# Performance work log

Hardware: AMD Instinct MI355X
Metric: run time of the kernel (lower is better)

## Reference

```python
import jax, jax.numpy as jnp
import numpy as np

N_NODES = 50000
N_EDGES = 800000
HIDDEN = 128
NUM_LAYERS = 3
NEG_SLOPE = 0.2  # PyG GATConv default leaky_relu slope


def setup_inputs() -> dict:
    key = jax.random.key(0)
    ks = jax.random.split(key, 10)
    d = HIDDEN
    glorot = 1.0 / np.sqrt(d)
    inp = {
        "x": jax.random.normal(ks[0], (N_NODES, d), dtype=jnp.float32),
        "edge_index": jax.random.randint(ks[1], (2, N_EDGES), 0, N_NODES, dtype=jnp.int32),
        "edge_mask": jax.random.uniform(ks[2], (N_EDGES,), dtype=jnp.float32),
        # GATConv params (heads=1)
        "W_gat": jax.random.normal(ks[3], (d, d), dtype=jnp.float32) * glorot,
        "a_src": jax.random.normal(ks[4], (d,), dtype=jnp.float32) * glorot,
        "a_dst": jax.random.normal(ks[5], (d,), dtype=jnp.float32) * glorot,
        "b_gat": jnp.zeros((d,), dtype=jnp.float32),
        # Stacked GCNConv params
        "W_gcn": jax.random.normal(ks[6], (NUM_LAYERS, d, d), dtype=jnp.float32) * glorot,
        "b_gcn": jnp.zeros((NUM_LAYERS, d), dtype=jnp.float32),
    }
    return inp


def _seg_softmax(e, seg, n):
    m = jax.ops.segment_max(e, seg, num_segments=n)
    p = jnp.exp(e - m[seg])
    s = jax.ops.segment_sum(p, seg, num_segments=n)
    return p / s[seg]


def reference(x, edge_index, edge_mask, W_gat, a_src, a_dst, b_gat, W_gcn, b_gcn):
    N = x.shape[0]
    loops = jnp.arange(N, dtype=edge_index.dtype)
    src = jnp.concatenate([edge_index[0], loops])  # [E+N] with self loops
    dst = jnp.concatenate([edge_index[1], loops])

    # --- GATConv (heads=1, add_self_loops=True); edge_attr ignored (edge_dim=None) ---
    xp = x @ W_gat                                      # [N, d]
    e = jax.nn.leaky_relu((xp @ a_src)[src] + (xp @ a_dst)[dst], NEG_SLOPE)
    alpha = _seg_softmax(e, dst, N)                     # segment softmax over incoming edges
    h = jax.ops.segment_sum(alpha[:, None] * xp[src], dst, num_segments=N) + b_gat

    # --- GCN normalization with edge_mask as edge_weight (self-loop weight = 1) ---
    w = jnp.concatenate([edge_mask, jnp.ones((N,), dtype=edge_mask.dtype)])
    deg = jax.ops.segment_sum(w, dst, num_segments=N)
    dinv = jnp.where(deg > 0, jax.lax.rsqrt(jnp.maximum(deg, 1e-12)), 0.0)
    norm = dinv[src] * w * dinv[dst]                    # [E+N]

    outs = [h]
    for l in range(NUM_LAYERS):
        z = outs[-1] @ W_gcn[l]                         # [N, d]
        z = jax.ops.segment_sum(norm[:, None] * z[src], dst, num_segments=N) + b_gcn[l]
        outs.append(jax.nn.relu(z))

    # JumpingKnowledge 'max': elementwise max over layer outputs
    return jnp.max(jnp.stack(outs, axis=0), axis=0)
```

## Files before the change

### kernel.cpp

```cpp
#include <hip/hip_runtime.h>

#define HIDDEN 128
#define NEG_SLOPE 0.2f
#define P_SORT 256

typedef unsigned short ushort_t;
typedef __attribute__((ext_vector_type(8))) short short8;
typedef __attribute__((ext_vector_type(4))) float floatx4;

static inline size_t align_up(size_t x, size_t a){ return (x + a - 1) & ~(a - 1); }

__device__ __forceinline__ ushort_t f2b(float f){
  unsigned u = __float_as_uint(f);
  unsigned r = (u + 0x7FFFu + ((u >> 16) & 1u)) >> 16;
  return (ushort_t)r;
}

__device__ __forceinline__ float b2f(ushort_t u){
  return __uint_as_float(((unsigned)u) << 16);
}

__device__ __forceinline__ void fma8(float* acc, uint4 v, float a){
  acc[0] += a * __uint_as_float(v.x << 16);
  acc[1] += a * __uint_as_float(v.x & 0xFFFF0000u);
  acc[2] += a * __uint_as_float(v.y << 16);
  acc[3] += a * __uint_as_float(v.y & 0xFFFF0000u);
  acc[4] += a * __uint_as_float(v.z << 16);
  acc[5] += a * __uint_as_float(v.z & 0xFFFF0000u);
  acc[6] += a * __uint_as_float(v.w << 16);
  acc[7] += a * __uint_as_float(v.w & 0xFFFF0000u);
}

__device__ __forceinline__ uint4 pack8(const float* f){
  uint4 u;
  u.x = (unsigned)f2b(f[0]) | ((unsigned)f2b(f[1]) << 16);
  u.y = (unsigned)f2b(f[2]) | ((unsigned)f2b(f[3]) << 16);
  u.z = (unsigned)f2b(f[4]) | ((unsigned)f2b(f[5]) << 16);
  u.w = (unsigned)f2b(f[6]) | ((unsigned)f2b(f[7]) << 16);
  return u;
}


__global__ __launch_bounds__(256) void k_b1cnt(const int* __restrict__ dst,
                                               int* __restrict__ bcnt,
                                               int E, int epb, int nbkt){
  __shared__ unsigned c[256];
  int t = threadIdx.x;
  c[t] = 0;
  __syncthreads();
  int e0 = blockIdx.x * epb;
  int e1 = min(E, e0 + epb);
  for (int e = e0 + t; e < e1; e += 256) atomicAdd(&c[dst[e] >> 8], 1u);
  __syncthreads();
  if (t < nbkt) bcnt[t * P_SORT + blockIdx.x] = (int)c[t];
}

__global__ void k_scan1(const int* __restrict__ in, int* __restrict__ incl,
                        int* __restrict__ blockSums, int M){
  __shared__ int sd[256];
  int t = threadIdx.x;
  int i = blockIdx.x*256 + t;
  int v = (i < M) ? in[i] : 0;
  sd[t] = v; __syncthreads();
  for (int off = 1; off < 256; off <<= 1){
    int add = (t >= off) ? sd[t-off] : 0;
    __syncthreads();
    sd[t] += add;
    __syncthreads();
  }
  if (i < M) incl[i] = sd[t];
  if (t == 255) blockSums[blockIdx.x] = sd[255];
}

__global__ void k_scan2(const int* __restrict__ blockSums, int* __restrict__ blockOffs, int nb){
  __shared__ int sd[256];
  __shared__ int carry;
  int t = threadIdx.x;
  if (t == 0) carry = 0;
  __syncthreads();
  for (int base = 0; base < nb; base += 256){
    int i = base + t;
    int v = (i < nb) ? blockSums[i] : 0;
    sd[t] = v; __syncthreads();
    for (int off = 1; off < 256; off <<= 1){
      int add = (t >= off) ? sd[t-off] : 0;
      __syncthreads();
      sd[t] += add;
      __syncthreads();
    }
    if (i < nb) blockOffs[i] = carry + sd[t] - v;
    __syncthreads();
    if (t == 0) carry += sd[255];
    __syncthreads();
  }
}

__global__ __launch_bounds__(256) void k_b1place(const int* __restrict__ src,
                                                 const int* __restrict__ dst,
                                                 const float* __restrict__ w,
                                                 const int* __restrict__ incl,
                                                 const int* __restrict__ bcnt,
                                                 const int* __restrict__ blockOffs,
                                                 int2* __restrict__ tpw,
                                                 int E, int epb, int nbkt){
  __shared__ int base_[256];
  __shared__ unsigned c[256];
  int t = threadIdx.x;
  c[t] = 0;
  if (t < nbkt){
    int idx = t * P_SORT + blockIdx.x;
    base_[t] = incl[idx] - bcnt[idx] + blockOffs[t];
  }
  __syncthreads();
  int e0 = blockIdx.x * epb;
  int e1 = min(E, e0 + epb);
  for (int e = e0 + t; e < e1; e += 256){
    int d = dst[e];
    int b = d >> 8;
    unsigned r = atomicAdd(&c[b], 1u);
    int pos = base_[b] + (int)r;
    tpw[pos] = make_int2((int)((unsigned)src[e] | ((unsigned)(d & 255) << 16)),
                         __float_as_int(w[e]));
  }
}

__global__ __launch_bounds__(256) void k_b2(const int2* __restrict__ tpw,
                                            const int* __restrict__ blockOffs,
                                            int2* __restrict__ col_sw,
                                            int* __restrict__ rowp,
                                            float* __restrict__ dinv,
                                            int N, int E, int nbkt){
  __shared__ int cnt[4096];
  __shared__ int tsum[256];
  __shared__ float wsum[256];
  int b = blockIdx.x, t = threadIdx.x;
  int e0 = blockOffs[b];
  int e1 = (b + 1 < nbkt) ? blockOffs[b + 1] : E;
  #pragma unroll
  for (int i = 0; i < 16; i++) cnt[t*16 + i] = 0;
  wsum[t] = 0.f;
  __syncthreads();
  for (int e = e0 + t; e < e1; e += 256){
    int2 pw = tpw[e];
    unsigned dl = ((unsigned)pw.x >> 16) & 255u;
    unsigned s  = ((unsigned)pw.x & 0xFFFFu) >> 12;
    atomicAdd(&cnt[(dl << 4) | s], 1);
  }
  __syncthreads();
  int loc[16]; int run = 0;
  #pragma unroll
  for (int i = 0; i < 16; i++){ loc[i] = run; run += cnt[t*16 + i]; }
  tsum[t] = run;
  __syncthreads();
  for (int off = 1; off < 256; off <<= 1){
    int add = (t >= off) ? tsum[t-off] : 0;
    __syncthreads();
    tsum[t] += add;
    __syncthreads();
  }
  int base = tsum[t] - run;
  #pragma unroll
  for (int i = 0; i < 16; i++) cnt[t*16 + i] = base + loc[i];
  int node = b*256 + t;
  if (node < N) rowp[node] = e0 + base;
  if (b == 0 && t == 0) rowp[N] = E;
  __syncthreads();
  for (int e = e0 + t; e < e1; e += 256){
    int2 pw = tpw[e];
    unsigned dl = ((unsigned)pw.x >> 16) & 255u;
    unsigned srcv = (unsigned)pw.x & 0xFFFFu;
    unsigned s = srcv >> 12;
    int pos = e0 + atomicAdd(&cnt[(dl << 4) | s], 1);
    col_sw[pos] = make_int2((int)srcv, pw.y);
    atomicAdd(&wsum[dl], __int_as_float(pw.y));
  }
  __syncthreads();
  if (node < N) dinv[node] = rsqrtf(wsum[t] + 1.0f);
}


__global__ void k_cast_w(const float* __restrict__ Wg, const float* __restrict__ Wc,
                         ushort_t* __restrict__ Wt){
  int i = blockIdx.x*256 + threadIdx.x;
  int mat = i >> 14, idx = i & 16383;
  int k = idx >> 7, n = idx & 127;
  float v = (mat == 0) ? Wg[idx] : Wc[(mat-1)*16384 + idx];
  Wt[mat*16384 + n*128 + k] = f2b(v);
}

__global__ __launch_bounds__(128) void k_gemm1(const float* __restrict__ Ain,
                                               const ushort_t* __restrict__ Wt,
                                               ushort_t* __restrict__ C,
                                               const float* __restrict__ a_src,
                                               const float* __restrict__ a_dst,
                                               const float* __restrict__ dinv,
                                               float2* __restrict__ attr,
                                               float* __restrict__ sdst, int M){
  int wave = threadIdx.x >> 6, l = threadIdx.x & 63;
  int q = l >> 4, lm = l & 15;
  int rowBase = blockIdx.x*64 + wave*32;
  floatx4 acc[2][8];
  #pragma unroll
  for (int mt = 0; mt < 2; mt++)
    #pragma unroll
    for (int nt = 0; nt < 8; nt++) acc[mt][nt] = (floatx4){0.f,0.f,0.f,0.f};

  #pragma unroll
  for (int kc = 0; kc < 4; kc++){
    int k0 = kc*32 + q*8;
    short8 a[2];
    #pragma unroll
    for (int mt = 0; mt < 2; mt++){
      long r = rowBase + mt*16 + lm;
      if (r < M){
        const float* ap = Ain + r*128 + k0;
        float4 u = *(const float4*)ap;
        float4 v = *(const float4*)(ap + 4);
        short8 tv;
        tv[0]=(short)f2b(u.x); tv[1]=(short)f2b(u.y); tv[2]=(short)f2b(u.z); tv[3]=(short)f2b(u.w);
        tv[4]=(short)f2b(v.x); tv[5]=(short)f2b(v.y); tv[6]=(short)f2b(v.z); tv[7]=(short)f2b(v.w);
        a[mt] = tv;
      } else a[mt] = (short8){0,0,0,0,0,0,0,0};
    }
    #pragma unroll
    for (int nt = 0; nt < 8; nt++){
      short8 b = *(const short8*)(Wt + (nt*16 + lm)*128 + k0);
      acc[0][nt] = __builtin_amdgcn_mfma_f32_16x16x32_bf16(a[0], b, acc[0][nt], 0, 0, 0);
      acc[1][nt] = __builtin_amdgcn_mfma_f32_16x16x32_bf16(a[1], b, acc[1][nt], 0, 0, 0);
    }
  }
  #pragma unroll
  for (int mt = 0; mt < 2; mt++){
    #pragma unroll
    for (int r = 0; r < 4; r++){
      long row = rowBase + mt*16 + q*4 + r;
      if (row < M){
        #pragma unroll
        for (int nt = 0; nt < 8; nt++)
          C[row*128 + nt*16 + lm] = f2b(acc[mt][nt][r]);
      }
    }
  }
  float as8[8], ad8[8];
  #pragma unroll
  for (int nt = 0; nt < 8; nt++){ as8[nt] = a_src[nt*16 + lm]; ad8[nt] = a_dst[nt*16 + lm]; }
  #pragma unroll
  for (int mt = 0; mt < 2; mt++){
    #pragma unroll
    for (int r = 0; r < 4; r++){
      float ps = 0.f, pd = 0.f;
      #pragma unroll
      for (int nt = 0; nt < 8; nt++){
        ps += acc[mt][nt][r] * as8[nt];
        pd += acc[mt][nt][r] * ad8[nt];
      }
      #pragma unroll
      for (int off = 1; off <= 8; off <<= 1){
        ps += __shfl_xor(ps, off, 64);
        pd += __shfl_xor(pd, off, 64);
      }
      long row = rowBase + mt*16 + q*4 + r;
      if (lm == 0 && row < M){
        attr[row] = make_float2(ps, dinv[row]);
        sdst[row] = pd;
      }
    }
  }
}

__global__ __launch_bounds__(256) void k_agg0(const ushort_t* __restrict__ feat,
                                              const int* __restrict__ rowp,
                                              const int2* __restrict__ col_sw,
                                              int2* __restrict__ col_en,
                                              int2* __restrict__ col_ea,
                                              const float2* __restrict__ attr,
                                              const float* __restrict__ sdst_,
                                              const float* __restrict__ bias,
                                              ushort_t* __restrict__ out, int N){
  int n = blockIdx.x*4 + (threadIdx.x >> 6);
  if (n >= N) return;
  int l = threadIdx.x & 63;
  int rs = rowp[n], re = rowp[n+1];
  float2 an = attr[n];
  float sdd = sdst_[n];
  float es = an.x + sdd;
  es = (es >= 0.f) ? es : NEG_SLOPE*es;
  float pself = __expf(es);
  float ps = 0.f;
  for (int j = rs + l; j < re; j += 64){
    int2 sw = col_sw[j];
    float w = __int_as_float(sw.y);
    float2 a = attr[sw.x];
    col_en[j] = make_int2(sw.x, __float_as_int(a.y * w * an.y));
    float ee = a.x + sdd;
    ee = (ee >= 0.f) ? ee : NEG_SLOPE*ee;
    float pe = __expf(ee);
    ps += pe;
    col_ea[j] = make_int2(sw.x, __float_as_int(pe));
  }
  #pragma unroll
  for (int off = 32; off >= 1; off >>= 1) ps += __shfl_xor(ps, off, 64);
  float inv = 1.f / (ps + pself);

  int sub = l >> 4, q = l & 15;
  const uint4* f16 = (const uint4*)feat;
  float acc[8] = {0.f,0.f,0.f,0.f,0.f,0.f,0.f,0.f};
  for (int base = rs; base < re; base += 24){
    int2 p[6]; float a[6];
    #pragma unroll
    for (int j = 0; j < 6; j++){
      int e = base + sub + 4*j;
      int cc = min(e, re-1);
      p[j] = col_ea[cc];
      a[j] = (e < re) ? __int_as_float(p[j].y) : 0.f;
    }
    uint4 v[6];
    #pragma unroll
    for (int j = 0; j < 6; j++) v[j] = f16[(size_t)p[j].x*16 + q];
    #pragma unroll
    for (int j = 0; j < 6; j++) fma8(acc, v[j], a[j]);
  }
  #pragma unroll
  for (int j = 0; j < 8; j++){
    acc[j] += __shfl_xor(acc[j], 16, 64);
    acc[j] += __shfl_xor(acc[j], 32, 64);
  }
  if (sub == 0){
    #pragma unroll
    for (int j = 0; j < 8; j++) acc[j] *= inv;
    uint4 v = f16[(size_t)n*16 + q];
    fma8(acc, v, pself * inv);
    float4 b0 = ((const float4*)bias)[q*2];
    float4 b1 = ((const float4*)bias)[q*2 + 1];
    acc[0]+=b0.x; acc[1]+=b0.y; acc[2]+=b0.z; acc[3]+=b0.w;
    acc[4]+=b1.x; acc[5]+=b1.y; acc[6]+=b1.z; acc[7]+=b1.w;
    ((uint4*)out)[(size_t)n*16 + q] = pack8(acc);
  }
}

template<int MODE>
__global__ __launch_bounds__(256) void k_fagg(const ushort_t* __restrict__ feat,
                                              const int* __restrict__ rowp,
                                              const int2* __restrict__ col_en,
                                              const float* __restrict__ dinv,
                                              const ushort_t* __restrict__ Wl,
                                              const float* __restrict__ bias,
                                              ushort_t* __restrict__ out,
                                              const ushort_t* __restrict__ j0,
                                              const ushort_t* __restrict__ j1,
                                              const ushort_t* __restrict__ j2,
                                              float* __restrict__ yout, int N){
  __shared__ ushort_t At[16][136];
  int wave = threadIdx.x >> 6, l = threadIdx.x & 63;
  int sub = l >> 4, q = l & 15;
  const uint4* f16 = (const uint4*)feat;
  int tile = blockIdx.x * 16;

  for (int i = 0; i < 4; i++){
    int row = wave*4 + i;
    int n = tile + row;
    int rs = 0, re = 0;
    if (n < N){ rs = rowp[n]; re = rowp[n+1]; }
    float acc[8] = {0.f,0.f,0.f,0.f,0.f,0.f,0.f,0.f};
    for (int base = rs; base < re; base += 24){
      int2 p[6]; float a[6];
      #pragma unroll
      for (int j = 0; j < 6; j++){
        int e = base + sub + 4*j;
        int cc = min(e, re-1);
        p[j] = col_en[cc];
        a[j] = (e < re) ? __int_as_float(p[j].y) : 0.f;
      }
      uint4 v[6];
      #pragma unroll
      for (int j = 0; j < 6; j++) v[j] = f16[(size_t)p[j].x*16 + q];
      #pragma unroll
      for (int j = 0; j < 6; j++) fma8(acc, v[j], a[j]);
    }
    #pragma unroll
    for (int j = 0; j < 8; j++){
      acc[j] += __shfl_xor(acc[j], 16, 64);
      acc[j] += __shfl_xor(acc[j], 32, 64);
    }
    if (sub == 0){
      if (n < N){
        float di = dinv[n];
        uint4 v = f16[(size_t)n*16 + q];
        fma8(acc, v, di*di);
      }
      *(uint4*)&At[row][q*8] = pack8(acc);
    }
  }
  __syncthreads();

  floatx4 co[2];
  co[0] = (floatx4){0.f,0.f,0.f,0.f};
  co[1] = (floatx4){0.f,0.f,0.f,0.f};
  #pragma unroll
  for (int kc = 0; kc < 4; kc++){
    int k0 = kc*32 + sub*8;
    short8 a = *(const short8*)&At[q][k0];
    #pragma unroll
    for (int ntl = 0; ntl < 2; ntl++){
      int nt = wave*2 + ntl;
      short8 b = *(const short8*)(Wl + (size_t)(nt*16 + q)*128 + k0);
      co[ntl] = __builtin_amdgcn_mfma_f32_16x16x32_bf16(a, b, co[ntl], 0, 0, 0);
    }
  }
  #pragma unroll
  for (int r = 0; r < 4; r++){
    int row = sub*4 + r;
    int node = tile + row;
    if (node < N){
      #pragma unroll
      for (int ntl = 0; ntl < 2; ntl++){
        int colg = wave*32 + ntl*16 + q;
        float v = co[ntl][r] + bias[colg];
        v = fmaxf(v, 0.f);
        size_t idx = (size_t)node*128 + colg;
        if (MODE == 1){
          out[idx] = f2b(v);
        } else {
          float m = fmaxf(fmaxf(b2f(j0[idx]), b2f(j1[idx])),
                          fmaxf(b2f(j2[idx]), v));
          yout[idx] = m;
        }
      }
    }
  }
}

extern "C" void kernel_launch(void* const* d_in, const int* in_sizes, int n_in,
                              void* d_out, int out_size, void* d_ws, size_t ws_size,
                              hipStream_t stream){
  const float* x      = (const float*)d_in[0];
  const int*   eidx   = (const int*)d_in[1];
  const float* emask  = (const float*)d_in[2];
  const float* W_gat  = (const float*)d_in[3];
  const float* a_src  = (const float*)d_in[4];
  const float* a_dst  = (const float*)d_in[5];
  const float* b_gat  = (const float*)d_in[6];
  const float* W_gcn  = (const float*)d_in[7];
  const float* b_gcn  = (const float*)d_in[8];
  int N = in_sizes[0] / HIDDEN;
  int E = in_sizes[1] / 2;
  const int* src = eidx;
  const int* dst = eidx + E;

  char* p = (char*)d_ws;
  auto carve = [&](size_t bytes)->char*{ char* q = p; p += align_up(bytes, 512); return q; };
  ushort_t* zb   = (ushort_t*)carve((size_t)N*HIDDEN*2);
  ushort_t* h0   = (ushort_t*)carve((size_t)N*HIDDEN*2);
  ushort_t* h1   = (ushort_t*)carve((size_t)N*HIDDEN*2);
  ushort_t* h2   = (ushort_t*)carve((size_t)N*HIDDEN*2);
  ushort_t* Wt   = (ushort_t*)carve((size_t)4*HIDDEN*HIDDEN*2);
  float2* attr   = (float2*)carve((size_t)N*8);
  float* sdst    = (float*)carve((size_t)N*4);
  float* dinv    = (float*)carve((size_t)N*4);
  int*   rowp    = (int*)  carve((size_t)(N+1)*4);
  int2*  col_sw  = (int2*) carve((size_t)E*8);
  int2*  col_en  = (int2*) carve((size_t)E*8);
  int2*  col_ea  = (int2*) carve((size_t)E*8);
  int2*  tpw     = (int2*) carve((size_t)E*8);
  int nbkt = (N + 255) >> 8;
  int M    = nbkt * P_SORT;
  int*   bcnt  = (int*)carve((size_t)M*4);
  int*   incl  = (int*)carve((size_t)M*4);
  int nbs = (M + 255) / 256;
  int*   blockSums = (int*)carve((size_t)nbs*4);
  int*   blockOffs = (int*)carve((size_t)nbs*4);
  (void)ws_size; (void)n_in; (void)out_size;

  int epb = (E + P_SORT - 1) / P_SORT;
  int gb  = (N + 63) / 64;
  int nwb = (N + 3) / 4;
  int nfb = (N + 15) / 16;

  k_b1cnt  <<<P_SORT, 256, 0, stream>>>(dst, bcnt, E, epb, nbkt);
  k_scan1  <<<nbs, 256, 0, stream>>>(bcnt, incl, blockSums, M);
  k_scan2  <<<1,   256, 0, stream>>>(blockSums, blockOffs, nbs);
  k_b1place<<<P_SORT, 256, 0, stream>>>(src, dst, emask, incl, bcnt, blockOffs,
                                        tpw, E, epb, nbkt);
  k_b2     <<<nbkt, 256, 0, stream>>>(tpw, blockOffs, col_sw, rowp, dinv, N, E, nbkt);

  k_cast_w<<<(4*HIDDEN*HIDDEN)/256, 256, 0, stream>>>(W_gat, W_gcn, Wt);

  k_gemm1<<<gb, 128, 0, stream>>>(x, Wt, zb, a_src, a_dst, dinv, attr, sdst, N);

  k_agg0<<<nwb, 256, 0, stream>>>(zb, rowp, col_sw, col_en, col_ea, attr, sdst,
                                  b_gat, h0, N);

  k_fagg<1><<<nfb, 256, 0, stream>>>(h0, rowp, col_en, dinv, Wt + (size_t)1*16384,
                                     b_gcn + 0, h1,
                                     nullptr, nullptr, nullptr, nullptr, N);
  k_fagg<1><<<nfb, 256, 0, stream>>>(h1, rowp, col_en, dinv, Wt + (size_t)2*16384,
                                     b_gcn + 128, h2,
                                     nullptr, nullptr, nullptr, nullptr, N);
  k_fagg<2><<<nfb, 256, 0, stream>>>(h2, rowp, col_en, dinv, Wt + (size_t)3*16384,
                                     b_gcn + 256, nullptr,
                                     h0, h1, h2, (float*)d_out, N);
}
```

Baseline: 340.6 us.

## Quantize gathered node features to int8 with per-row scales for aggregation

Node feature tables that are gathered per edge (the GAT projection and each GCN layer's input) are stored as int8 with a per-row float scale instead of bf16. The scale is folded into the edge weights, so the gather reads half the bytes. The precomputed col_en edge array is dropped: GCN edge weights are rebuilt on the fly from col_sw and the per-node scale, which also folds in dinv. This trades extra scale loads and LDS staging against lower gather bandwidth, and adds quantization error that may break the accuracy tolerance.

Result: slower. 392.8 us (+15.3%).

```diff
diff --git a/kernel.cpp b/kernel.cpp
--- a/kernel.cpp
+++ b/kernel.cpp
@@ -20,15 +20,30 @@
   return __uint_as_float(((unsigned)u) << 16);
 }
 
-__device__ __forceinline__ void fma8(float* acc, uint4 v, float a){
-  acc[0] += a * __uint_as_float(v.x << 16);
-  acc[1] += a * __uint_as_float(v.x & 0xFFFF0000u);
-  acc[2] += a * __uint_as_float(v.y << 16);
-  acc[3] += a * __uint_as_float(v.y & 0xFFFF0000u);
-  acc[4] += a * __uint_as_float(v.z << 16);
-  acc[5] += a * __uint_as_float(v.z & 0xFFFF0000u);
-  acc[6] += a * __uint_as_float(v.w << 16);
-  acc[7] += a * __uint_as_float(v.w & 0xFFFF0000u);
+__device__ __forceinline__ void fma8q(float* acc, uint2 v, float a){
+  int x = (int)v.x, y = (int)v.y;
+  acc[0] += a * (float)((x << 24) >> 24);
+  acc[1] += a * (float)((x << 16) >> 24);
+  acc[2] += a * (float)((x <<  8) >> 24);
+  acc[3] += a * (float)( x        >> 24);
+  acc[4] += a * (float)((y << 24) >> 24);
+  acc[5] += a * (float)((y << 16) >> 24);
+  acc[6] += a * (float)((y <<  8) >> 24);
+  acc[7] += a * (float)( y        >> 24);
+}
+
+__device__ __forceinline__ uint2 packq8(const float* f, float qi){
+  unsigned a = 0, b = 0;
+  int q;
+  q = (int)rintf(f[0]*qi); a |= ((unsigned)q & 255u);
+  q = (int)rintf(f[1]*qi); a |= ((unsigned)q & 255u) << 8;
+  q = (int)rintf(f[2]*qi); a |= ((unsigned)q & 255u) << 16;
+  q = (int)rintf(f[3]*qi); a |= ((unsigned)q & 255u) << 24;
+  q = (int)rintf(f[4]*qi); b |= ((unsigned)q & 255u);
+  q = (int)rintf(f[5]*qi); b |= ((unsigned)q & 255u) << 8;
+  q = (int)rintf(f[6]*qi); b |= ((unsigned)q & 255u) << 16;
+  q = (int)rintf(f[7]*qi); b |= ((unsigned)q & 255u) << 24;
+  uint2 r; r.x = a; r.y = b; return r;
 }
 
 __device__ __forceinline__ uint4 pack8(const float* f){
@@ -190,12 +205,15 @@
 
 __global__ __launch_bounds__(128) void k_gemm1(const float* __restrict__ Ain,
                                                const ushort_t* __restrict__ Wt,
-                                               ushort_t* __restrict__ C,
+                                               unsigned* __restrict__ zq,
+                                               float* __restrict__ sc_z,
                                                const float* __restrict__ a_src,
                                                const float* __restrict__ a_dst,
                                                const float* __restrict__ dinv,
                                                float2* __restrict__ attr,
                                                float* __restrict__ sdst, int M){
+  __shared__ uint4 zq8v[64][8];
+  char (*zq8)[128] = (char(*)[128])zq8v;
   int wave = threadIdx.x >> 6, l = threadIdx.x & 63;
   int q = l >> 4, lm = l & 15;
   int rowBase = blockIdx.x*64 + wave*32;
@@ -233,12 +251,18 @@
   for (int mt = 0; mt < 2; mt++){
     #pragma unroll
     for (int r = 0; r < 4; r++){
+      float rm = 0.f;
+      #pragma unroll
+      for (int nt = 0; nt < 8; nt++) rm = fmaxf(rm, fabsf(acc[mt][nt][r]));
+      #pragma unroll
+      for (int off = 1; off <= 8; off <<= 1) rm = fmaxf(rm, __shfl_xor(rm, off, 64));
+      float qi = (rm > 0.f) ? 127.f/rm : 0.f;
+      int lrow = wave*32 + mt*16 + q*4 + r;
+      #pragma unroll
+      for (int nt = 0; nt < 8; nt++)
+        zq8[lrow][nt*16 + lm] = (char)(int)rintf(acc[mt][nt][r]*qi);
       long row = rowBase + mt*16 + q*4 + r;
-      if (row < M){
-        #pragma unroll
-        for (int nt = 0; nt < 8; nt++)
-          C[row*128 + nt*16 + lm] = f2b(acc[mt][nt][r]);
-      }
+      if (lm == 0 && row < M) sc_z[row] = rm * (1.f/127.f);
     }
   }
   float as8[8], ad8[8];
@@ -266,17 +290,30 @@
       }
     }
   }
-}
-
-__global__ __launch_bounds__(256) void k_agg0(const ushort_t* __restrict__ feat,
+  __syncthreads();
+  {
+    int t = threadIdx.x;
+    int lrow = t >> 1, half = t & 1;
+    long row = (long)blockIdx.x*64 + lrow;
+    if (row < M){
+      uint4* dq = (uint4*)zq + row*8 + half*4;
+      #pragma unroll
+      for (int k = 0; k < 4; k++) dq[k] = zq8v[lrow][half*4 + k];
+    }
+  }
+}
+
+__global__ __launch_bounds__(256) void k_agg0(const unsigned* __restrict__ zq,
+                                              const float* __restrict__ sc_z,
                                               const int* __restrict__ rowp,
                                               const int2* __restrict__ col_sw,
-                                              int2* __restrict__ col_en,
                                               int2* __restrict__ col_ea,
                                               const float2* __restrict__ attr,
                                               const float* __restrict__ sdst_,
                                               const float* __restrict__ bias,
-                                              ushort_t* __restrict__ out, int N){
+                                              ushort_t* __restrict__ out,
+                                              unsigned* __restrict__ g0,
+                                              float* __restrict__ scd0, int N){
   int n = blockIdx.x*4 + (threadIdx.x >> 6);
   if (n >= N) return;
   int l = threadIdx.x & 63;
@@ -289,21 +326,19 @@
   float ps = 0.f;
   for (int j = rs + l; j < re; j += 64){
     int2 sw = col_sw[j];
-    float w = __int_as_float(sw.y);
     float2 a = attr[sw.x];
-    col_en[j] = make_int2(sw.x, __float_as_int(a.y * w * an.y));
     float ee = a.x + sdd;
     ee = (ee >= 0.f) ? ee : NEG_SLOPE*ee;
     float pe = __expf(ee);
     ps += pe;
-    col_ea[j] = make_int2(sw.x, __float_as_int(pe));
+    col_ea[j] = make_int2(sw.x, __float_as_int(pe * sc_z[sw.x]));
   }
   #pragma unroll
   for (int off = 32; off >= 1; off >>= 1) ps += __shfl_xor(ps, off, 64);
   float inv = 1.f / (ps + pself);
 
   int sub = l >> 4, q = l & 15;
-  const uint4* f16 = (const uint4*)feat;
+  const uint2* f8 = (const uint2*)zq;
   float acc[8] = {0.f,0.f,0.f,0.f,0.f,0.f,0.f,0.f};
   for (int base = rs; base < re; base += 24){
     int2 p[6]; float a[6];
@@ -314,11 +349,11 @@
       p[j] = col_ea[cc];
       a[j] = (e < re) ? __int_as_float(p[j].y) : 0.f;
     }
-    uint4 v[6];
-    #pragma unroll
-    for (int j = 0; j < 6; j++) v[j] = f16[(size_t)p[j].x*16 + q];
-    #pragma unroll
-    for (int j = 0; j < 6; j++) fma8(acc, v[j], a[j]);
+    uint2 v[6];
+    #pragma unroll
+    for (int j = 0; j < 6; j++) v[j] = f8[(size_t)p[j].x*16 + q];
+    #pragma unroll
+    for (int j = 0; j < 6; j++) fma8q(acc, v[j], a[j]);
   }
   #pragma unroll
   for (int j = 0; j < 8; j++){
@@ -328,39 +363,52 @@
   if (sub == 0){
     #pragma unroll
     for (int j = 0; j < 8; j++) acc[j] *= inv;
-    uint4 v = f16[(size_t)n*16 + q];
-    fma8(acc, v, pself * inv);
+    fma8q(acc, f8[(size_t)n*16 + q], pself * inv * sc_z[n]);
     float4 b0 = ((const float4*)bias)[q*2];
     float4 b1 = ((const float4*)bias)[q*2 + 1];
     acc[0]+=b0.x; acc[1]+=b0.y; acc[2]+=b0.z; acc[3]+=b0.w;
     acc[4]+=b1.x; acc[5]+=b1.y; acc[6]+=b1.z; acc[7]+=b1.w;
     ((uint4*)out)[(size_t)n*16 + q] = pack8(acc);
+    float rm = 0.f;
+    #pragma unroll
+    for (int j = 0; j < 8; j++) rm = fmaxf(rm, fabsf(acc[j]));
+    #pragma unroll
+    for (int off = 1; off <= 8; off <<= 1) rm = fmaxf(rm, __shfl_xor(rm, off, 64));
+    float qi = (rm > 0.f) ? 127.f/rm : 0.f;
+    ((uint2*)g0)[(size_t)n*16 + q] = packq8(acc, qi);
+    if (l == 0) scd0[n] = rm * (1.f/127.f) * an.y;
   }
 }
 
 template<int MODE>
-__global__ __launch_bounds__(256) void k_fagg(const ushort_t* __restrict__ feat,
+__global__ __launch_bounds__(256) void k_fagg(const unsigned* __restrict__ gin,
+                                              const float* __restrict__ scd_prev,
                                               const int* __restrict__ rowp,
-                                              const int2* __restrict__ col_en,
+                                              const int2* __restrict__ col_sw,
                                               const float* __restrict__ dinv,
                                               const ushort_t* __restrict__ Wl,
                                               const float* __restrict__ bias,
                                               ushort_t* __restrict__ out,
+                                              unsigned* __restrict__ gout,
+                                              float* __restrict__ scd_out,
                                               const ushort_t* __restrict__ j0,
                                               const ushort_t* __restrict__ j1,
                                               const ushort_t* __restrict__ j2,
                                               float* __restrict__ yout, int N){
   __shared__ ushort_t At[16][136];
+  __shared__ uint4 q8v[16][8];
+  __shared__ unsigned rmaxs[16];
+  char (*q8s)[128] = (char(*)[128])q8v;
   int wave = threadIdx.x >> 6, l = threadIdx.x & 63;
   int sub = l >> 4, q = l & 15;
-  const uint4* f16 = (const uint4*)feat;
+  const uint2* f8 = (const uint2*)gin;
   int tile = blockIdx.x * 16;
 
   for (int i = 0; i < 4; i++){
     int row = wave*4 + i;
     int n = tile + row;
-    int rs = 0, re = 0;
-    if (n < N){ rs = rowp[n]; re = rowp[n+1]; }
+    int rs = 0, re = 0; float dn = 0.f, sprev = 0.f;
+    if (n < N){ rs = rowp[n]; re = rowp[n+1]; dn = dinv[n]; sprev = scd_prev[n]; }
     float acc[8] = {0.f,0.f,0.f,0.f,0.f,0.f,0.f,0.f};
     for (int base = rs; base < re; base += 24){
       int2 p[6]; float a[6];
@@ -368,14 +416,14 @@
       for (int j = 0; j < 6; j++){
         int e = base + sub + 4*j;
         int cc = min(e, re-1);
-        p[j] = col_en[cc];
-        a[j] = (e < re) ? __int_as_float(p[j].y) : 0.f;
-      }
-      uint4 v[6];
-      #pragma unroll
-      for (int j = 0; j < 6; j++) v[j] = f16[(size_t)p[j].x*16 + q];
-      #pragma unroll
-      for (int j = 0; j < 6; j++) fma8(acc, v[j], a[j]);
+        p[j] = col_sw[cc];
+        a[j] = (e < re) ? __int_as_float(p[j].y) * scd_prev[p[j].x] : 0.f;
+      }
+      uint2 v[6];
+      #pragma unroll
+      for (int j = 0; j < 6; j++) v[j] = f8[(size_t)p[j].x*16 + q];
+      #pragma unroll
+      for (int j = 0; j < 6; j++) fma8q(acc, v[j], a[j]);
     }
     #pragma unroll
     for (int j = 0; j < 8; j++){
@@ -383,14 +431,13 @@
       acc[j] += __shfl_xor(acc[j], 32, 64);
     }
     if (sub == 0){
-      if (n < N){
-        float di = dinv[n];
-        uint4 v = f16[(size_t)n*16 + q];
-        fma8(acc, v, di*di);
-      }
+      if (n < N) fma8q(acc, f8[(size_t)n*16 + q], sprev);
+      #pragma unroll
+      for (int j = 0; j < 8; j++) acc[j] *= dn;
       *(uint4*)&At[row][q*8] = pack8(acc);
     }
   }
+  if (threadIdx.x < 16) rmaxs[threadIdx.x] = 0u;
   __syncthreads();
 
   floatx4 co[2];
@@ -407,16 +454,20 @@
       co[ntl] = __builtin_amdgcn_mfma_f32_16x16x32_bf16(a, b, co[ntl], 0, 0, 0);
     }
   }
+  float vv[4][2];
   #pragma unroll
   for (int r = 0; r < 4; r++){
     int row = sub*4 + r;
     int node = tile + row;
-    if (node < N){
-      #pragma unroll
-      for (int ntl = 0; ntl < 2; ntl++){
-        int colg = wave*32 + ntl*16 + q;
-        float v = co[ntl][r] + bias[colg];
-        v = fmaxf(v, 0.f);
+    float lmax = 0.f;
+    #pragma unroll
+    for (int ntl = 0; ntl < 2; ntl++){
+      int colg = wave*32 + ntl*16 + q;
+      float v = co[ntl][r] + bias[colg];
+      v = fmaxf(v, 0.f);
+      vv[r][ntl] = v;
+      lmax = fmaxf(lmax, v);
+      if (node < N){
         size_t idx = (size_t)node*128 + colg;
         if (MODE == 1){
           out[idx] = f2b(v);
@@ -426,6 +477,34 @@
           yout[idx] = m;
         }
       }
+    }
+    if (MODE == 1) atomicMax(&rmaxs[row], __float_as_uint(lmax));
+  }
+  if (MODE == 1){
+    __syncthreads();
+    #pragma unroll
+    for (int r = 0; r < 4; r++){
+      int row = sub*4 + r;
+      float rm = __uint_as_float(rmaxs[row]);
+      float qi = (rm > 0.f) ? 127.f/rm : 0.f;
+      #pragma unroll
+      for (int ntl = 0; ntl < 2; ntl++){
+        int colg = wave*32 + ntl*16 + q;
+        q8s[row][colg] = (char)(int)rintf(vv[r][ntl]*qi);
+      }
+    }
+    if (threadIdx.x < 16){
+      int node = tile + threadIdx.x;
+      if (node < N){
+        float rm = __uint_as_float(rmaxs[threadIdx.x]);
+        scd_out[node] = rm * (1.f/127.f) * dinv[node];
+      }
+    }
+    __syncthreads();
+    if (threadIdx.x < 128){
+      int row = threadIdx.x >> 3, c = threadIdx.x & 7;
+      int node = tile + row;
+      if (node < N) ((uint4*)gout)[(size_t)node*8 + c] = q8v[row][c];
     }
   }
 }
@@ -449,17 +528,23 @@
 
   char* p = (char*)d_ws;
   auto carve = [&](size_t bytes)->char*{ char* q = p; p += align_up(bytes, 512); return q; };
-  ushort_t* zb   = (ushort_t*)carve((size_t)N*HIDDEN*2);
   ushort_t* h0   = (ushort_t*)carve((size_t)N*HIDDEN*2);
   ushort_t* h1   = (ushort_t*)carve((size_t)N*HIDDEN*2);
   ushort_t* h2   = (ushort_t*)carve((size_t)N*HIDDEN*2);
   ushort_t* Wt   = (ushort_t*)carve((size_t)4*HIDDEN*HIDDEN*2);
+  unsigned* zq   = (unsigned*)carve((size_t)N*HIDDEN);
+  unsigned* g0q  = (unsigned*)carve((size_t)N*HIDDEN);
+  unsigned* g1q  = (unsigned*)carve((size_t)N*HIDDEN);
+  unsigned* g2q  = (unsigned*)carve((size_t)N*HIDDEN);
+  float* sc_z    = (float*)carve((size_t)N*4);
+  float* scd0    = (float*)carve((size_t)N*4);
+  float* scd1    = (float*)carve((size_t)N*4);
+  float* scd2    = (float*)carve((size_t)N*4);
   float2* attr   = (float2*)carve((size_t)N*8);
   float* sdst    = (float*)carve((size_t)N*4);
   float* dinv    = (float*)carve((size_t)N*4);
   int*   rowp    = (int*)  carve((size_t)(N+1)*4);
   int2*  col_sw  = (int2*) carve((size_t)E*8);
-  int2*  col_en  = (int2*) carve((size_t)E*8);
   int2*  col_ea  = (int2*) carve((size_t)E*8);
   int2*  tpw     = (int2*) carve((size_t)E*8);
   int nbkt = (N + 255) >> 8;
@@ -485,18 +570,21 @@
 
   k_cast_w<<<(4*HIDDEN*HIDDEN)/256, 256, 0, stream>>>(W_gat, W_gcn, Wt);
 
-  k_gemm1<<<gb, 128, 0, stream>>>(x, Wt, zb, a_src, a_dst, dinv, attr, sdst, N);
-
-  k_agg0<<<nwb, 256, 0, stream>>>(zb, rowp, col_sw, col_en, col_ea, attr, sdst,
-                                  b_gat, h0, N);
-
-  k_fagg<1><<<nfb, 256, 0, stream>>>(h0, rowp, col_en, dinv, Wt + (size_t)1*16384,
-                                     b_gcn + 0, h1,
+  k_gemm1<<<gb, 128, 0, stream>>>(x, Wt, zq, sc_z, a_src, a_dst, dinv, attr, sdst, N);
+
+  k_agg0<<<nwb, 256, 0, stream>>>(zq, sc_z, rowp, col_sw, col_ea, attr, sdst,
+                                  b_gat, h0, g0q, scd0, N);
+
+  k_fagg<1><<<nfb, 256, 0, stream>>>(g0q, scd0, rowp, col_sw, dinv,
+                                     Wt + (size_t)1*16384, b_gcn + 0,
+                                     h1, g1q, scd1,
                                      nullptr, nullptr, nullptr, nullptr, N);
-  k_fagg<1><<<nfb, 256, 0, stream>>>(h1, rowp, col_en, dinv, Wt + (size_t)2*16384,
-                                     b_gcn + 128, h2,
+  k_fagg<1><<<nfb, 256, 0, stream>>>(g1q, scd1, rowp, col_sw, dinv,
+                                     Wt + (size_t)2*16384, b_gcn + 128,
+                                     h2, g2q, scd2,
                                      nullptr, nullptr, nullptr, nullptr, N);
-  k_fagg<2><<<nfb, 256, 0, stream>>>(h2, rowp, col_en, dinv, Wt + (size_t)3*16384,
-                                     b_gcn + 256, nullptr,
+  k_fagg<2><<<nfb, 256, 0, stream>>>(g2q, scd2, rowp, col_sw, dinv,
+                                     Wt + (size_t)3*16384, b_gcn + 256,
+                                     nullptr, nullptr, nullptr,
                                      h0, h1, h2, (float*)d_out, N);
 }
```
